# Kernel optimization log

Hardware: AMD Instinct MI355X
Metric: run time of the kernel (lower is better)

The kernel has to match this reference:

```python
import jax, jax.numpy as jnp
import numpy as np

B, N, D_IN = 4, 2048, 128
H, HD = 4, 32  # num_heads, head_dim (out_features=128, concat=True)
NEG_SLOPE = 0.2


def setup_inputs() -> dict:
    key = jax.random.key(0)
    kx, kadj, kw, ka = jax.random.split(key, 4)
    x = jax.random.normal(kx, (B, N, D_IN), dtype=jnp.float32)
    adj_mx = jax.random.randint(kadj, (N, N), 0, 2, dtype=jnp.int32)
    # xavier-uniform-ish scaling for params
    W = jax.random.normal(kw, (H * HD, D_IN), dtype=jnp.float32) * (1.0 / np.sqrt(D_IN))
    a = jax.random.normal(ka, (H, 2 * HD, 1), dtype=jnp.float32) * (1.0 / np.sqrt(2 * HD))
    return {"x": x, "adj_mx": adj_mx, "W": W, "a": a}


def reference(x, adj_mx, W, a):
    # x: (B,N,D_in); W: (H*hd, D_in) [nn.Linear weight]; a: (H, 2*hd, 1)
    b, n, _ = x.shape
    hd = a.shape[1] // 2
    h = (x @ W.T).reshape(b, n, H, hd)  # (B,N,H,hd)
    # e_ij = a^T [h_i || h_j] = a1.h_i + a2.h_j  (exact decomposition of the concat-matmul)
    a1 = a[:, :hd, 0]  # (H, hd)
    a2 = a[:, hd:, 0]  # (H, hd)
    ei = jnp.einsum('bnhd,hd->bnh', h, a1)
    ej = jnp.einsum('bnhd,hd->bnh', h, a2)
    e = ei[:, :, None, :] + ej[:, None, :, :]  # (B,N,N,H)
    e = jnp.where(e > 0, e, NEG_SLOPE * e)  # leaky_relu(0.2)
    mask = (adj_mx == 0)[None, :, :, None]  # (1,N,N,1)
    e = jnp.where(mask, -jnp.inf, e)
    attn = jax.nn.softmax(e, axis=2)  # softmax over neighbors j
    # dropout p=0.0 (inference) -> identity
    out = jnp.einsum('bijh,bjhd->bihd', attn, h)  # (B,N,H,hd)
    return out.reshape(b, n, H * hd)  # concat heads
```

## Files before the change

### kernel.cpp

```cpp
#include <hip/hip_runtime.h>
#include <hip/hip_bf16.h>
#include <stdint.h>

#define B 4
#define N 2048
#define DIN 128
#define H 4
#define HD 32
#define NEG 0.2f

typedef __attribute__((ext_vector_type(8))) short short8;
typedef __attribute__((ext_vector_type(4))) float f32x4;

__global__ __launch_bounds__(256) void k_gemm(const float* __restrict__ x,
                                              const float* __restrict__ W,
                                              const float* __restrict__ a,
                                              unsigned short* __restrict__ VT,
                                              float* __restrict__ ei_t,
                                              float* __restrict__ ej_t) {
    __shared__ float Wt0[64][64];
    __shared__ float Wt1[64][64];
    __shared__ float xT[64][20];
    const int tid = threadIdx.x;
    const int lane = tid & 63;
    const int r0 = (tid >> 6) * 4;
    const int c2 = lane;
    const int rowBase = blockIdx.x * 16;
    float acc[4][2];
#pragma unroll
    for (int i = 0; i < 4; ++i) { acc[i][0] = 0.f; acc[i][1] = 0.f; }

    for (int kh = 0; kh < 2; ++kh) {
        __syncthreads();
        {
            const int c = tid & 127;
            const int qb = (tid >> 7) * 8;
            const int ci = c >> 1, pl = c & 1;
            const float4* W4 = (const float4*)W;
#pragma unroll
            for (int q = 0; q < 8; ++q) {
                float4 v = W4[c * 32 + kh * 16 + qb + q];
                int kk = (qb + q) * 4;
                if (pl == 0) {
                    Wt0[kk + 0][ci] = v.x; Wt0[kk + 1][ci] = v.y;
                    Wt0[kk + 2][ci] = v.z; Wt0[kk + 3][ci] = v.w;
                } else {
                    Wt1[kk + 0][ci] = v.x; Wt1[kk + 1][ci] = v.y;
                    Wt1[kk + 2][ci] = v.z; Wt1[kk + 3][ci] = v.w;
                }
            }
        }
        {
            const int rl = tid >> 4;
            const int q = tid & 15;
            float4 v = ((const float4*)x)[(rowBase + rl) * 32 + kh * 16 + q];
            int kk = q * 4;
            xT[kk + 0][rl] = v.x; xT[kk + 1][rl] = v.y;
            xT[kk + 2][rl] = v.z; xT[kk + 3][rl] = v.w;
        }
        __syncthreads();
#pragma unroll 8
        for (int kk = 0; kk < 64; ++kk) {
            float w0 = Wt0[kk][c2];
            float w1 = Wt1[kk][c2];
#pragma unroll
            for (int i = 0; i < 4; ++i) {
                float xv = xT[kk][r0 + i];
                acc[i][0] += xv * w0;
                acc[i][1] += xv * w1;
            }
        }
    }

    const int c0 = 2 * c2;
    const int head = c0 >> 5, d0 = c0 & 31;
    const int b = rowBase >> 11;
    const int n0 = (rowBase & 2047) + r0;
    const int bh = b * 4 + head;

    {
        ushort4 p0, p1;
        unsigned short* q0 = (unsigned short*)&p0;
        unsigned short* q1 = (unsigned short*)&p1;
#pragma unroll
        for (int i = 0; i < 4; ++i) {
            __hip_bfloat16 h0 = __float2bfloat16(acc[i][0]);
            __hip_bfloat16 h1 = __float2bfloat16(acc[i][1]);
            q0[i] = *(unsigned short*)&h0;
            q1[i] = *(unsigned short*)&h1;
        }
        *(ushort4*)&VT[((size_t)bh * 32 + d0) * 2048 + n0] = p0;
        *(ushort4*)&VT[((size_t)bh * 32 + d0 + 1) * 2048 + n0] = p1;
    }
    {
        float a10 = a[head * 64 + d0],      a11 = a[head * 64 + d0 + 1];
        float a20 = a[head * 64 + 32 + d0], a21 = a[head * 64 + 32 + d0 + 1];
#pragma unroll
        for (int i = 0; i < 4; ++i) {
            float pi = acc[i][0] * a10 + acc[i][1] * a11;
            float pj = acc[i][0] * a20 + acc[i][1] * a21;
#pragma unroll
            for (int off = 1; off < 16; off <<= 1) {
                pi += __shfl_xor(pi, off);
                pj += __shfl_xor(pj, off);
            }
            if ((lane & 15) == 0) {
                ei_t[(size_t)bh * 2048 + n0 + i] = pi;
                ej_t[(size_t)bh * 2048 + n0 + i] = pj;
            }
        }
    }
}

__global__ __launch_bounds__(256) void k_pack(const int* __restrict__ adj,
                                              unsigned long long* __restrict__ bits) {
    int t = blockIdx.x * 256 + threadIdx.x;
    int v = adj[t];
    unsigned long long m = __ballot(v != 0);
    if ((threadIdx.x & 63) == 0) bits[t >> 6] = m;
}

__global__ __launch_bounds__(512) void k_attn_g(const unsigned short* __restrict__ VT,
                                                const float* __restrict__ ei_t,
                                                const float* __restrict__ ej_t,
                                                const unsigned long long* __restrict__ bits,
                                                float* __restrict__ out) {
    __shared__ float red[4][64][13];

    const int tid = threadIdx.x;
    const int bid = blockIdx.x;
    const int rt = bid & 31;
    const int head = (bid >> 5) & 3;
    const int b = bid >> 7;
    const int wv = tid >> 6, lane = tid & 63;
    const int wtile = wv & 3, par = wv >> 2;
    const int lr = lane & 15;
    const int g = lane >> 4;
    const int rowW = rt * 64 + wtile * 16;
    const int bh = b * 4 + head;

    const unsigned short* V0 = VT + (size_t)bh * 32 * 2048 + (size_t)lr * 2048;
    const unsigned short* V1 = V0 + 16 * 2048;
    const float* ejp = ej_t + (size_t)bh * 2048;
    const float eir = ei_t[(size_t)bh * 2048 + rowW + lr];
    const unsigned long long* mrow = bits + (size_t)(rowW + lr) * (N / 64);

    f32x4 acc0 = {0.f, 0.f, 0.f, 0.f};
    f32x4 acc1 = {0.f, 0.f, 0.f, 0.f};
    f32x4 accS = {0.f, 0.f, 0.f, 0.f};
    short8 onesb;
    {
        short ov = (lr == 0) ? (short)0x3F80 : (short)0;
#pragma unroll
        for (int e = 0; e < 8; ++e) onesb[e] = ov;
    }

    for (int jc = par * 64; jc < N; jc += 128) {
        const unsigned long long word = mrow[jc >> 6];
#pragma unroll
        for (int ks = 0; ks < 2; ++ks) {
            const int joff = jc + ks * 32 + g * 8;
            float4 ea = *(const float4*)(ejp + joff);
            float4 eb = *(const float4*)(ejp + joff + 4);
            short8 b0 = *(const short8*)(V0 + joff);
            short8 b1 = *(const short8*)(V1 + joff);
            const unsigned int mb = (unsigned int)(word >> (ks * 32 + g * 8)) & 0xffu;
            float ej8[8] = {ea.x, ea.y, ea.z, ea.w, eb.x, eb.y, eb.z, eb.w};
            short8 pa;
#pragma unroll
            for (int e = 0; e < 8; ++e) {
                float s = eir + ej8[e];
                float el = fmaxf(s, NEG * s);
                float p = ((mb >> e) & 1u) ? __expf(el) : 0.f;
                __hip_bfloat16 pb = __float2bfloat16(p);
                pa[e] = (short)*(unsigned short*)&pb;
            }
            acc0 = __builtin_amdgcn_mfma_f32_16x16x32_bf16(pa, b0, acc0, 0, 0, 0);
            acc1 = __builtin_amdgcn_mfma_f32_16x16x32_bf16(pa, b1, acc1, 0, 0, 0);
            accS = __builtin_amdgcn_mfma_f32_16x16x32_bf16(pa, onesb, accS, 0, 0, 0);
        }
    }

    if (par == 1) {
        float* r = &red[wtile][lane][0];
#pragma unroll
        for (int q = 0; q < 4; ++q) {
            r[q] = acc0[q]; r[4 + q] = acc1[q]; r[8 + q] = accS[q];
        }
    }
    __syncthreads();
    if (par == 0) {
        const float* r = &red[wtile][lane][0];
#pragma unroll
        for (int q = 0; q < 4; ++q) {
            acc0[q] += r[q]; acc1[q] += r[4 + q]; accS[q] += r[8 + q];
        }
#pragma unroll
        for (int reg = 0; reg < 4; ++reg) {
            const float sr = __shfl(accS[reg], g * 16);
            const float inv = 1.f / sr;
            const int m = 4 * g + reg;
            float* dst = &out[(size_t)(b * N + rowW + m) * 128 + head * 32 + lr];
            dst[0]  = acc0[reg] * inv;
            dst[16] = acc1[reg] * inv;
        }
    }
}

__global__ __launch_bounds__(256) void k_fused(const float* __restrict__ x,
                                               const int* __restrict__ adj,
                                               const float* __restrict__ W,
                                               const float* __restrict__ a,
                                               float* __restrict__ out) {
    __shared__ float Ws[32][129];
    __shared__ float xs[64][132];
    __shared__ float hs[64][44];
    __shared__ float ejs[64];
    __shared__ float eis[128];
    __shared__ float a1s[32], a2s[32];
    __shared__ unsigned long long mb[128];

    const int tid = threadIdx.x;
    const int bid = blockIdx.x;
    const int rt = bid & 15;
    const int head = (bid >> 4) & 3;
    const int b = bid >> 6;
    const int row0 = rt * 128;

    for (int idx = tid; idx < 32 * 128; idx += 256) {
        int d = idx >> 7, k = idx & 127;
        Ws[d][k] = W[(head * 32 + d) * 128 + k];
    }
    if (tid < 32) a1s[tid] = a[head * 64 + tid];
    else if (tid < 64) a2s[tid - 32] = a[head * 64 + tid];
    __syncthreads();

    for (int c0 = 0; c0 < 128; c0 += 64) {
        __syncthreads();
        {
            int jj = tid >> 2, k0 = (tid & 3) * 32;
            const float4* src = (const float4*)&x[(b * N + row0 + c0 + jj) * 128 + k0];
#pragma unroll
            for (int q = 0; q < 8; ++q) *(float4*)&xs[jj][k0 + q * 4] = src[q];
        }
        __syncthreads();
        {
            int jj = tid >> 2, db = (tid & 3) * 8;
#pragma unroll
            for (int dd = 0; dd < 8; ++dd) {
                float s = 0.f;
                for (int k = 0; k < 128; ++k) s += xs[jj][k] * Ws[db + dd][k];
                hs[jj][db + dd] = s;
            }
        }
        __syncthreads();
        if (tid < 64) {
            float s = 0.f;
#pragma unroll
            for (int d = 0; d < 32; ++d) s += hs[tid][d] * a1s[d];
            eis[c0 + tid] = s;
        }
    }

    const int dgrp = tid & 3, d0 = dgrp * 8;
    const int rseg = tid >> 2;
    float acc[2][8];
    float sacc[2] = {0.f, 0.f};
#pragma unroll
    for (int k = 0; k < 2; ++k)
#pragma unroll
        for (int d = 0; d < 8; ++d) acc[k][d] = 0.f;

    for (int jc = 0; jc < N; jc += 64) {
        __syncthreads();
        {
            int jj = tid >> 2, k0 = (tid & 3) * 32;
            const float4* src = (const float4*)&x[(b * N + jc + jj) * 128 + k0];
#pragma unroll
            for (int q = 0; q < 8; ++q) *(float4*)&xs[jj][k0 + q * 4] = src[q];
        }
        {
            int wv = tid >> 6, lane = tid & 63;
            for (int p = 0; p < 32; ++p) {
                int il = p * 4 + wv;
                unsigned long long m = __ballot(adj[(row0 + il) * N + jc + lane] != 0);
                if (lane == 0) mb[il] = m;
            }
        }
        __syncthreads();
        {
            int jj = tid >> 2, db = (tid & 3) * 8;
#pragma unroll
            for (int dd = 0; dd < 8; ++dd) {
                float s = 0.f;
                for (int k = 0; k < 128; ++k) s += xs[jj][k] * Ws[db + dd][k];
                hs[jj][db + dd] = s;
            }
        }
        __syncthreads();
        if (tid < 64) {
            float s = 0.f;
#pragma unroll
            for (int d = 0; d < 32; ++d) s += hs[tid][d] * a2s[d];
            ejs[tid] = s;
        }
        __syncthreads();
        for (int jj = 0; jj < 64; ++jj) {
            float ejv = ejs[jj];
            float hv[8];
#pragma unroll
            for (int d = 0; d < 8; ++d) hv[d] = hs[jj][d0 + d];
#pragma unroll
            for (int k = 0; k < 2; ++k) {
                int il = rseg * 2 + k;
                float s = eis[il] + ejv;
                float el = s > 0.f ? s : NEG * s;
                float p = ((mb[il] >> jj) & 1ull) ? __expf(el) : 0.f;
                sacc[k] += p;
#pragma unroll
                for (int d = 0; d < 8; ++d) acc[k][d] += p * hv[d];
            }
        }
    }
#pragma unroll
    for (int k = 0; k < 2; ++k) {
        int il = rseg * 2 + k;
        float inv = 1.f / sacc[k];
        float* dst = &out[(b * N + row0 + il) * 128 + head * 32 + d0];
#pragma unroll
        for (int d = 0; d < 8; ++d) dst[d] = acc[k][d] * inv;
    }
}

extern "C" void kernel_launch(void* const* d_in, const int* in_sizes, int n_in,
                              void* d_out, int out_size, void* d_ws, size_t ws_size,
                              hipStream_t stream) {
    const float* x = nullptr; const int* adj = nullptr;
    const float* W = nullptr; const float* a = nullptr;
    for (int i = 0; i < n_in; ++i) {
        switch (in_sizes[i]) {
            case B * N * DIN:  x   = (const float*)d_in[i]; break;
            case N * N:        adj = (const int*)d_in[i];   break;
            case H * HD * DIN: W   = (const float*)d_in[i]; break;
            case H * 2 * HD:   a   = (const float*)d_in[i]; break;
        }
    }
    float* out = (float*)d_out;

    const size_t szVT = (size_t)B * H * HD * N * 2;
    const size_t szE  = (size_t)B * H * N * 4;
    const size_t szBits = (size_t)N * (N / 64) * 8;
    const size_t need = szVT + 2 * szE + szBits;

    if (ws_size >= need) {
        char* ws = (char*)d_ws;
        unsigned short* VT = (unsigned short*)ws;
        float* ei_t = (float*)(ws + szVT);
        float* ej_t = (float*)(ws + szVT + szE);
        unsigned long long* bits = (unsigned long long*)(ws + szVT + 2 * szE);

        k_gemm<<<512, 256, 0, stream>>>(x, W, a, VT, ei_t, ej_t);
        k_pack<<<(N * N) / 256, 256, 0, stream>>>(adj, bits);
        k_attn_g<<<512, 512, 0, stream>>>(VT, ei_t, ej_t, bits, out);
    } else {
        k_fused<<<256, 256, 0, stream>>>(x, adj, W, a, out);
    }
}
```

Before: 130.5 us.

## Split attention kernel over four j-partitions with register double-buffered loads and exp2

The attention kernel now gives each block 32 rows, using two row tiles times four j-partitions per 512-thread block, and launches twice as many blocks. The j loop is software-pipelined: the mask word and V tiles for the next chunk are loaded into registers while the current chunk is computed. ei/ej are pre-scaled by log2(e) in the GEMM kernel so the inner loop can use exp2 directly. The aim is more parallelism, hidden load latency and cheaper exponentials, at the cost of a larger three-way LDS reduction and extra register pressure.

New measurement: 130.1 us. No clear change (-0.3%).

```diff
diff --git a/kernel.cpp b/kernel.cpp
--- a/kernel.cpp
+++ b/kernel.cpp
@@ -8,6 +8,7 @@
 #define H 4
 #define HD 32
 #define NEG 0.2f
+#define LOG2E 1.4426950408889634f
 
 typedef __attribute__((ext_vector_type(8))) short short8;
 typedef __attribute__((ext_vector_type(4))) float f32x4;
@@ -105,8 +106,8 @@
                 pj += __shfl_xor(pj, off);
             }
             if ((lane & 15) == 0) {
-                ei_t[(size_t)bh * 2048 + n0 + i] = pi;
-                ej_t[(size_t)bh * 2048 + n0 + i] = pj;
+                ei_t[(size_t)bh * 2048 + n0 + i] = pi * LOG2E;
+                ej_t[(size_t)bh * 2048 + n0 + i] = pj * LOG2E;
             }
         }
     }
@@ -125,18 +126,18 @@
                                                 const float* __restrict__ ej_t,
                                                 const unsigned long long* __restrict__ bits,
                                                 float* __restrict__ out) {
-    __shared__ float red[4][64][13];
+    __shared__ float red[3][2][64][13];
 
     const int tid = threadIdx.x;
     const int bid = blockIdx.x;
-    const int rt = bid & 31;
-    const int head = (bid >> 5) & 3;
-    const int b = bid >> 7;
+    const int rt = bid & 63;
+    const int head = (bid >> 6) & 3;
+    const int b = bid >> 8;
     const int wv = tid >> 6, lane = tid & 63;
-    const int wtile = wv & 3, par = wv >> 2;
+    const int wtile = wv & 1, par = wv >> 1;
     const int lr = lane & 15;
     const int g = lane >> 4;
-    const int rowW = rt * 64 + wtile * 16;
+    const int rowW = rt * 32 + wtile * 16;
     const int bh = b * 4 + head;
 
     const unsigned short* V0 = VT + (size_t)bh * 32 * 2048 + (size_t)lr * 2048;
@@ -155,15 +156,23 @@
         for (int e = 0; e < 8; ++e) onesb[e] = ov;
     }
 
-    for (int jc = par * 64; jc < N; jc += 128) {
-        const unsigned long long word = mrow[jc >> 6];
+    const int jstart = par * 64;
+
+    auto LDC = [&](int jc, unsigned long long& w,
+                   short8& v00, short8& v10, short8& v01, short8& v11) {
+        w = mrow[jc >> 6];
+        v00 = *(const short8*)(V0 + jc + g * 8);
+        v10 = *(const short8*)(V1 + jc + g * 8);
+        v01 = *(const short8*)(V0 + jc + 32 + g * 8);
+        v11 = *(const short8*)(V1 + jc + 32 + g * 8);
+    };
+    auto CMP = [&](int jc, unsigned long long word,
+                   short8 v00, short8 v10, short8 v01, short8 v11) {
 #pragma unroll
         for (int ks = 0; ks < 2; ++ks) {
             const int joff = jc + ks * 32 + g * 8;
             float4 ea = *(const float4*)(ejp + joff);
             float4 eb = *(const float4*)(ejp + joff + 4);
-            short8 b0 = *(const short8*)(V0 + joff);
-            short8 b1 = *(const short8*)(V1 + joff);
             const unsigned int mb = (unsigned int)(word >> (ks * 32 + g * 8)) & 0xffu;
             float ej8[8] = {ea.x, ea.y, ea.z, ea.w, eb.x, eb.y, eb.z, eb.w};
             short8 pa;
@@ -171,18 +180,35 @@
             for (int e = 0; e < 8; ++e) {
                 float s = eir + ej8[e];
                 float el = fmaxf(s, NEG * s);
-                float p = ((mb >> e) & 1u) ? __expf(el) : 0.f;
+                float p = ((mb >> e) & 1u) ? __builtin_amdgcn_exp2f(el) : 0.f;
                 __hip_bfloat16 pb = __float2bfloat16(p);
                 pa[e] = (short)*(unsigned short*)&pb;
             }
-            acc0 = __builtin_amdgcn_mfma_f32_16x16x32_bf16(pa, b0, acc0, 0, 0, 0);
-            acc1 = __builtin_amdgcn_mfma_f32_16x16x32_bf16(pa, b1, acc1, 0, 0, 0);
+            short8 u0 = ks ? v01 : v00;
+            short8 u1 = ks ? v11 : v10;
+            acc0 = __builtin_amdgcn_mfma_f32_16x16x32_bf16(pa, u0, acc0, 0, 0, 0);
+            acc1 = __builtin_amdgcn_mfma_f32_16x16x32_bf16(pa, u1, acc1, 0, 0, 0);
             accS = __builtin_amdgcn_mfma_f32_16x16x32_bf16(pa, onesb, accS, 0, 0, 0);
         }
-    }
-
-    if (par == 1) {
-        float* r = &red[wtile][lane][0];
+    };
+
+    unsigned long long wA, wB;
+    short8 A00, A10, A01, A11, B00, B10, B01, B11;
+    int jc = jstart;
+    LDC(jc, wA, A00, A10, A01, A11);
+#pragma unroll 1
+    for (int it = 0; it < 4; ++it) {
+        int j1 = jc + 256; if (j1 >= N) j1 = jstart;
+        LDC(j1, wB, B00, B10, B01, B11);
+        CMP(jc, wA, A00, A10, A01, A11);
+        int j2 = j1 + 256; if (j2 >= N) j2 = jstart;
+        LDC(j2, wA, A00, A10, A01, A11);
+        CMP(j1, wB, B00, B10, B01, B11);
+        jc = j2;
+    }
+
+    if (par != 0) {
+        float* r = &red[par - 1][wtile][lane][0];
 #pragma unroll
         for (int q = 0; q < 4; ++q) {
             r[q] = acc0[q]; r[4 + q] = acc1[q]; r[8 + q] = accS[q];
@@ -190,10 +216,13 @@
     }
     __syncthreads();
     if (par == 0) {
-        const float* r = &red[wtile][lane][0];
-#pragma unroll
-        for (int q = 0; q < 4; ++q) {
-            acc0[q] += r[q]; acc1[q] += r[4 + q]; accS[q] += r[8 + q];
+#pragma unroll
+        for (int p = 0; p < 3; ++p) {
+            const float* r = &red[p][wtile][lane][0];
+#pragma unroll
+            for (int q = 0; q < 4; ++q) {
+                acc0[q] += r[q]; acc1[q] += r[4 + q]; accS[q] += r[8 + q];
+            }
         }
 #pragma unroll
         for (int reg = 0; reg < 4; ++reg) {
@@ -361,7 +390,7 @@
 
         k_gemm<<<512, 256, 0, stream>>>(x, W, a, VT, ei_t, ej_t);
         k_pack<<<(N * N) / 256, 256, 0, stream>>>(adj, bits);
-        k_attn_g<<<512, 512, 0, stream>>>(VT, ei_t, ej_t, bits, out);
+        k_attn_g<<<1024, 512, 0, stream>>>(VT, ei_t, ej_t, bits, out);
     } else {
         k_fused<<<256, 256, 0, stream>>>(x, adj, W, a, out);
     }
```

## Stage V and ej windows in LDS with double buffering and merge prep kernels

Applied to the files above, without the earlier changes.

Fuses the adjacency bit-pack kernel into the projection kernel as extra blocks, which removes one launch. The attention kernel now uses 128-row blocks (256 blocks) and stages 512-column windows of V (swizzled XOR layout written by the producer) and ej into double-buffered LDS. Global prefetch of the next window overlaps with MFMA compute, replacing per-wave direct global loads and the two-half partial reduction. The exponent is switched to exp2 with log2e folded into ei/ej. The trade-off is fewer blocks, which means lower parallelism on the large CU count.

Measured after the change: 111.7 us. -14.4%, faster.

```diff
diff --git a/kernel.cpp b/kernel.cpp
--- a/kernel.cpp
+++ b/kernel.cpp
@@ -8,20 +8,33 @@
 #define H 4
 #define HD 32
 #define NEG 0.2f
+#define LOG2E 1.4426950408889634f
+#define WINJ 512
 
 typedef __attribute__((ext_vector_type(8))) short short8;
 typedef __attribute__((ext_vector_type(4))) float f32x4;
 
-__global__ __launch_bounds__(256) void k_gemm(const float* __restrict__ x,
+__global__ __launch_bounds__(256) void k_prep(const float* __restrict__ x,
                                               const float* __restrict__ W,
                                               const float* __restrict__ a,
+                                              const int* __restrict__ adj,
                                               unsigned short* __restrict__ VT,
                                               float* __restrict__ ei_t,
-                                              float* __restrict__ ej_t) {
+                                              float* __restrict__ ej_t,
+                                              unsigned long long* __restrict__ bits) {
     __shared__ float Wt0[64][64];
     __shared__ float Wt1[64][64];
     __shared__ float xT[64][20];
+
     const int tid = threadIdx.x;
+    if (blockIdx.x >= 512) {
+        int t = (blockIdx.x - 512) * 256 + tid;
+        int v = adj[t];
+        unsigned long long m = __ballot(v != 0);
+        if ((tid & 63) == 0) bits[t >> 6] = m;
+        return;
+    }
+
     const int lane = tid & 63;
     const int r0 = (tid >> 6) * 4;
     const int c2 = lane;
@@ -89,8 +102,13 @@
             q0[i] = *(unsigned short*)&h0;
             q1[i] = *(unsigned short*)&h1;
         }
-        *(ushort4*)&VT[((size_t)bh * 32 + d0) * 2048 + n0] = p0;
-        *(ushort4*)&VT[((size_t)bh * 32 + d0 + 1) * 2048 + n0] = p1;
+        const int wdw = n0 >> 9;
+        const int gw  = (n0 >> 3) & 63;
+        const int off = n0 & 7;
+        const int gs0 = gw ^ (d0 & 7);
+        const int gs1 = gw ^ ((d0 + 1) & 7);
+        *(ushort4*)&VT[((size_t)bh * 32 + d0) * 2048 + wdw * WINJ + gs0 * 8 + off] = p0;
+        *(ushort4*)&VT[((size_t)bh * 32 + d0 + 1) * 2048 + wdw * WINJ + gs1 * 8 + off] = p1;
     }
     {
         float a10 = a[head * 64 + d0],      a11 = a[head * 64 + d0 + 1];
@@ -105,43 +123,34 @@
                 pj += __shfl_xor(pj, off);
             }
             if ((lane & 15) == 0) {
-                ei_t[(size_t)bh * 2048 + n0 + i] = pi;
-                ej_t[(size_t)bh * 2048 + n0 + i] = pj;
+                ei_t[(size_t)bh * 2048 + n0 + i] = pi * LOG2E;
+                ej_t[(size_t)bh * 2048 + n0 + i] = pj * LOG2E;
             }
         }
     }
 }
 
-__global__ __launch_bounds__(256) void k_pack(const int* __restrict__ adj,
-                                              unsigned long long* __restrict__ bits) {
-    int t = blockIdx.x * 256 + threadIdx.x;
-    int v = adj[t];
-    unsigned long long m = __ballot(v != 0);
-    if ((threadIdx.x & 63) == 0) bits[t >> 6] = m;
-}
-
-__global__ __launch_bounds__(512) void k_attn_g(const unsigned short* __restrict__ VT,
+__global__ __launch_bounds__(512) void k_attn_l(const unsigned short* __restrict__ VT,
                                                 const float* __restrict__ ei_t,
                                                 const float* __restrict__ ej_t,
                                                 const unsigned long long* __restrict__ bits,
                                                 float* __restrict__ out) {
-    __shared__ float red[4][64][13];
+    __shared__ unsigned short Vs[2][32 * WINJ];
+    __shared__ float ejs[2][WINJ];
 
     const int tid = threadIdx.x;
     const int bid = blockIdx.x;
-    const int rt = bid & 31;
-    const int head = (bid >> 5) & 3;
-    const int b = bid >> 7;
+    const int rt = bid & 15;
+    const int head = (bid >> 4) & 3;
+    const int b = bid >> 6;
     const int wv = tid >> 6, lane = tid & 63;
-    const int wtile = wv & 3, par = wv >> 2;
     const int lr = lane & 15;
     const int g = lane >> 4;
-    const int rowW = rt * 64 + wtile * 16;
+    const int rowW = rt * 128 + wv * 16;
     const int bh = b * 4 + head;
 
-    const unsigned short* V0 = VT + (size_t)bh * 32 * 2048 + (size_t)lr * 2048;
-    const unsigned short* V1 = V0 + 16 * 2048;
-    const float* ejp = ej_t + (size_t)bh * 2048;
+    const unsigned short* VTb = VT + (size_t)bh * 32 * 2048;
+    const float* ejg = ej_t + (size_t)bh * 2048;
     const float eir = ei_t[(size_t)bh * 2048 + rowW + lr];
     const unsigned long long* mrow = bits + (size_t)(rowW + lr) * (N / 64);
 
@@ -155,55 +164,89 @@
         for (int e = 0; e < 8; ++e) onesb[e] = ov;
     }
 
-    for (int jc = par * 64; jc < N; jc += 128) {
-        const unsigned long long word = mrow[jc >> 6];
-#pragma unroll
-        for (int ks = 0; ks < 2; ++ks) {
-            const int joff = jc + ks * 32 + g * 8;
-            float4 ea = *(const float4*)(ejp + joff);
-            float4 eb = *(const float4*)(ejp + joff + 4);
-            short8 b0 = *(const short8*)(V0 + joff);
-            short8 b1 = *(const short8*)(V1 + joff);
-            const unsigned int mb = (unsigned int)(word >> (ks * 32 + g * 8)) & 0xffu;
-            float ej8[8] = {ea.x, ea.y, ea.z, ea.w, eb.x, eb.y, eb.z, eb.w};
-            short8 pa;
-#pragma unroll
-            for (int e = 0; e < 8; ++e) {
-                float s = eir + ej8[e];
-                float el = fmaxf(s, NEG * s);
-                float p = ((mb >> e) & 1u) ? __expf(el) : 0.f;
-                __hip_bfloat16 pb = __float2bfloat16(p);
-                pa[e] = (short)*(unsigned short*)&pb;
-            }
-            acc0 = __builtin_amdgcn_mfma_f32_16x16x32_bf16(pa, b0, acc0, 0, 0, 0);
-            acc1 = __builtin_amdgcn_mfma_f32_16x16x32_bf16(pa, b1, acc1, 0, 0, 0);
-            accS = __builtin_amdgcn_mfma_f32_16x16x32_bf16(pa, onesb, accS, 0, 0, 0);
-        }
-    }
-
-    if (par == 1) {
-        float* r = &red[wtile][lane][0];
-#pragma unroll
-        for (int q = 0; q < 4; ++q) {
-            r[q] = acc0[q]; r[4 + q] = acc1[q]; r[8 + q] = accS[q];
+    {
+#pragma unroll
+        for (int i = 0; i < 4; ++i) {
+            int L = i * 512 + tid, d = L >> 6, gr = L & 63;
+            float4 v = *(const float4*)&VTb[(size_t)d * 2048 + gr * 8];
+            *(float4*)&Vs[0][(size_t)L * 8] = v;
+        }
+        if (tid < 128) {
+            float4 e = *(const float4*)&ejg[tid * 4];
+            *(float4*)&ejs[0][tid * 4] = e;
         }
     }
     __syncthreads();
-    if (par == 0) {
-        const float* r = &red[wtile][lane][0];
-#pragma unroll
-        for (int q = 0; q < 4; ++q) {
-            acc0[q] += r[q]; acc1[q] += r[4 + q]; accS[q] += r[8 + q];
-        }
-#pragma unroll
-        for (int reg = 0; reg < 4; ++reg) {
-            const float sr = __shfl(accS[reg], g * 16);
-            const float inv = 1.f / sr;
-            const int m = 4 * g + reg;
-            float* dst = &out[(size_t)(b * N + rowW + m) * 128 + head * 32 + lr];
-            dst[0]  = acc0[reg] * inv;
-            dst[16] = acc1[reg] * inv;
-        }
+
+    for (int w = 0; w < 4; ++w) {
+        const int buf = w & 1;
+        float4 vr0, vr1, vr2, vr3, er;
+        const bool pf = (w < 3);
+        if (pf) {
+            const unsigned short* src = VTb + (w + 1) * WINJ;
+            int L0 = tid,        d0_ = L0 >> 6, g0_ = L0 & 63;
+            int L1 = 512 + tid,  d1_ = L1 >> 6, g1_ = L1 & 63;
+            int L2 = 1024 + tid, d2_ = L2 >> 6, g2_ = L2 & 63;
+            int L3 = 1536 + tid, d3_ = L3 >> 6, g3_ = L3 & 63;
+            vr0 = *(const float4*)&src[(size_t)d0_ * 2048 + g0_ * 8];
+            vr1 = *(const float4*)&src[(size_t)d1_ * 2048 + g1_ * 8];
+            vr2 = *(const float4*)&src[(size_t)d2_ * 2048 + g2_ * 8];
+            vr3 = *(const float4*)&src[(size_t)d3_ * 2048 + g3_ * 8];
+            if (tid < 128) er = *(const float4*)&ejg[(w + 1) * WINJ + tid * 4];
+        }
+        __builtin_amdgcn_sched_barrier(0);
+
+        const unsigned short* Vb = &Vs[buf][0];
+        const float* ejb = &ejs[buf][0];
+#pragma unroll 4
+        for (int jl = 0; jl < WINJ; jl += 64) {
+            const unsigned long long word = mrow[(w * WINJ + jl) >> 6];
+#pragma unroll
+            for (int ks = 0; ks < 2; ++ks) {
+                const int G = (jl >> 3) + ks * 4 + g;
+                const int gs = (G ^ (lr & 7)) * 8;
+                short8 b0 = *(const short8*)&Vb[lr * WINJ + gs];
+                short8 b1 = *(const short8*)&Vb[(16 + lr) * WINJ + gs];
+                const int f = jl + ks * 32 + g * 8;
+                float4 ea = *(const float4*)&ejb[f];
+                float4 eb = *(const float4*)&ejb[f + 4];
+                const unsigned int mb =
+                    (unsigned int)(word >> (ks * 32 + g * 8)) & 0xffu;
+                float ej8[8] = {ea.x, ea.y, ea.z, ea.w, eb.x, eb.y, eb.z, eb.w};
+                short8 pa;
+#pragma unroll
+                for (int e = 0; e < 8; ++e) {
+                    float s = eir + ej8[e];
+                    float el = fmaxf(s, NEG * s);
+                    float p = ((mb >> e) & 1u) ? __builtin_amdgcn_exp2f(el) : 0.f;
+                    __hip_bfloat16 pb = __float2bfloat16(p);
+                    pa[e] = (short)*(unsigned short*)&pb;
+                }
+                acc0 = __builtin_amdgcn_mfma_f32_16x16x32_bf16(pa, b0, acc0, 0, 0, 0);
+                acc1 = __builtin_amdgcn_mfma_f32_16x16x32_bf16(pa, b1, acc1, 0, 0, 0);
+                accS = __builtin_amdgcn_mfma_f32_16x16x32_bf16(pa, onesb, accS, 0, 0, 0);
+            }
+        }
+
+        if (pf) {
+            const int nbuf = buf ^ 1;
+            *(float4*)&Vs[nbuf][(size_t)tid * 8]          = vr0;
+            *(float4*)&Vs[nbuf][(size_t)(512 + tid) * 8]  = vr1;
+            *(float4*)&Vs[nbuf][(size_t)(1024 + tid) * 8] = vr2;
+            *(float4*)&Vs[nbuf][(size_t)(1536 + tid) * 8] = vr3;
+            if (tid < 128) *(float4*)&ejs[nbuf][tid * 4] = er;
+        }
+        __syncthreads();
+    }
+
+#pragma unroll
+    for (int reg = 0; reg < 4; ++reg) {
+        const float sr = __shfl(accS[reg], g * 16);
+        const float inv = 1.f / sr;
+        const int m = 4 * g + reg;
+        float* dst = &out[(size_t)(b * N + rowW + m) * 128 + head * 32 + lr];
+        dst[0]  = acc0[reg] * inv;
+        dst[16] = acc1[reg] * inv;
     }
 }
 
@@ -359,9 +402,8 @@
         float* ej_t = (float*)(ws + szVT + szE);
         unsigned long long* bits = (unsigned long long*)(ws + szVT + 2 * szE);
 
-        k_gemm<<<512, 256, 0, stream>>>(x, W, a, VT, ei_t, ej_t);
-        k_pack<<<(N * N) / 256, 256, 0, stream>>>(adj, bits);
-        k_attn_g<<<512, 512, 0, stream>>>(VT, ei_t, ej_t, bits, out);
+        k_prep<<<512 + (N * N) / 256, 256, 0, stream>>>(x, W, a, adj, VT, ei_t, ej_t, bits);
+        k_attn_l<<<256, 512, 0, stream>>>(VT, ei_t, ej_t, bits, out);
     } else {
         k_fused<<<256, 256, 0, stream>>>(x, adj, W, a, out);
     }
```

## Fuse adjacency packing into GEMM, tile V layout, prefetch V fragments

Applied to the files above, without the earlier changes.

Merges the adjacency bit-packing kernel into the projection kernel as extra blocks, which saves one launch. V is now written through shared memory into a fragment-tiled layout so each MFMA operand is a contiguous 16-byte load, replacing the earlier strided rows. The attention loop software-prefetches the next iteration's V fragments and mask word. It also folds log2(e) into ei/ej so the kernel can use native exp2. The changes cost extra shared memory, registers and occupancy-hint constraints, and the loop is now hardcoded to 16 iterations.

New measurement: 116.1 us. -11.0%, faster.

```diff
diff --git a/kernel.cpp b/kernel.cpp
--- a/kernel.cpp
+++ b/kernel.cpp
@@ -8,20 +8,34 @@
 #define H 4
 #define HD 32
 #define NEG 0.2f
+#define LOG2E 1.4426950408889634f
 
 typedef __attribute__((ext_vector_type(8))) short short8;
 typedef __attribute__((ext_vector_type(4))) float f32x4;
 
-__global__ __launch_bounds__(256) void k_gemm(const float* __restrict__ x,
+
+__global__ __launch_bounds__(256) void k_prep(const float* __restrict__ x,
                                               const float* __restrict__ W,
                                               const float* __restrict__ a,
+                                              const int* __restrict__ adj,
                                               unsigned short* __restrict__ VT,
                                               float* __restrict__ ei_t,
-                                              float* __restrict__ ej_t) {
+                                              float* __restrict__ ej_t,
+                                              unsigned long long* __restrict__ bits) {
     __shared__ float Wt0[64][64];
     __shared__ float Wt1[64][64];
     __shared__ float xT[64][20];
+    __shared__ unsigned short Vl[16][128];
+
     const int tid = threadIdx.x;
+    if (blockIdx.x >= 512) {
+        int t = (blockIdx.x - 512) * 256 + tid;
+        int v = adj[t];
+        unsigned long long m = __ballot(v != 0);
+        if ((tid & 63) == 0) bits[t >> 6] = m;
+        return;
+    }
+
     const int lane = tid & 63;
     const int r0 = (tid >> 6) * 4;
     const int c2 = lane;
@@ -73,28 +87,26 @@
     }
 
     const int c0 = 2 * c2;
-    const int head = c0 >> 5, d0 = c0 & 31;
+    const int headT = c0 >> 5, d0 = c0 & 31;
     const int b = rowBase >> 11;
     const int n0 = (rowBase & 2047) + r0;
-    const int bh = b * 4 + head;
+    const int n0_blk = rowBase & 2047;
 
     {
-        ushort4 p0, p1;
-        unsigned short* q0 = (unsigned short*)&p0;
-        unsigned short* q1 = (unsigned short*)&p1;
+        unsigned int* Vl32 = (unsigned int*)&Vl[0][0];
 #pragma unroll
         for (int i = 0; i < 4; ++i) {
             __hip_bfloat16 h0 = __float2bfloat16(acc[i][0]);
             __hip_bfloat16 h1 = __float2bfloat16(acc[i][1]);
-            q0[i] = *(unsigned short*)&h0;
-            q1[i] = *(unsigned short*)&h1;
-        }
-        *(ushort4*)&VT[((size_t)bh * 32 + d0) * 2048 + n0] = p0;
-        *(ushort4*)&VT[((size_t)bh * 32 + d0 + 1) * 2048 + n0] = p1;
+            unsigned int v = (unsigned int)*(unsigned short*)&h0 |
+                             ((unsigned int)*(unsigned short*)&h1 << 16);
+            Vl32[(r0 + i) * 64 + c2] = v;
+        }
     }
     {
-        float a10 = a[head * 64 + d0],      a11 = a[head * 64 + d0 + 1];
-        float a20 = a[head * 64 + 32 + d0], a21 = a[head * 64 + 32 + d0 + 1];
+        float a10 = a[headT * 64 + d0],      a11 = a[headT * 64 + d0 + 1];
+        float a20 = a[headT * 64 + 32 + d0], a21 = a[headT * 64 + 32 + d0 + 1];
+        const int bh_e = b * 4 + headT;
 #pragma unroll
         for (int i = 0; i < 4; ++i) {
             float pi = acc[i][0] * a10 + acc[i][1] * a11;
@@ -105,26 +117,35 @@
                 pj += __shfl_xor(pj, off);
             }
             if ((lane & 15) == 0) {
-                ei_t[(size_t)bh * 2048 + n0 + i] = pi;
-                ej_t[(size_t)bh * 2048 + n0 + i] = pj;
-            }
-        }
+                ei_t[(size_t)bh_e * 2048 + n0 + i] = pi * LOG2E;
+                ej_t[(size_t)bh_e * 2048 + n0 + i] = pj * LOG2E;
+            }
+        }
+    }
+    __syncthreads();
+    {
+        const int d = tid >> 1, nh = tid & 1;
+        const int hd_ = d >> 5, d31 = d & 31;
+        const int bh = b * 4 + hd_;
+        const int gran = (n0_blk >> 3) + nh;
+        ushort4 o0, o1;
+        unsigned short* q = (unsigned short*)&o0;
+#pragma unroll
+        for (int k = 0; k < 4; ++k) q[k] = Vl[nh * 8 + k][d];
+        q = (unsigned short*)&o1;
+#pragma unroll
+        for (int k = 0; k < 4; ++k) q[k] = Vl[nh * 8 + 4 + k][d];
+        unsigned short* dst = &VT[((size_t)(bh * 256 + gran) * 32 + d31) * 8];
+        *(ushort4*)&dst[0] = o0;
+        *(ushort4*)&dst[4] = o1;
     }
 }
 
-__global__ __launch_bounds__(256) void k_pack(const int* __restrict__ adj,
-                                              unsigned long long* __restrict__ bits) {
-    int t = blockIdx.x * 256 + threadIdx.x;
-    int v = adj[t];
-    unsigned long long m = __ballot(v != 0);
-    if ((threadIdx.x & 63) == 0) bits[t >> 6] = m;
-}
-
-__global__ __launch_bounds__(512) void k_attn_g(const unsigned short* __restrict__ VT,
-                                                const float* __restrict__ ei_t,
-                                                const float* __restrict__ ej_t,
-                                                const unsigned long long* __restrict__ bits,
-                                                float* __restrict__ out) {
+__global__ __launch_bounds__(512, 4) void k_attn_c(const unsigned short* __restrict__ VT,
+                                                   const float* __restrict__ ei_t,
+                                                   const float* __restrict__ ej_t,
+                                                   const unsigned long long* __restrict__ bits,
+                                                   float* __restrict__ out) {
     __shared__ float red[4][64][13];
 
     const int tid = threadIdx.x;
@@ -139,8 +160,7 @@
     const int rowW = rt * 64 + wtile * 16;
     const int bh = b * 4 + head;
 
-    const unsigned short* V0 = VT + (size_t)bh * 32 * 2048 + (size_t)lr * 2048;
-    const unsigned short* V1 = V0 + 16 * 2048;
+    const unsigned short* VTb = VT + (size_t)bh * 256 * 32 * 8;
     const float* ejp = ej_t + (size_t)bh * 2048;
     const float eir = ei_t[(size_t)bh * 2048 + rowW + lr];
     const unsigned long long* mrow = bits + (size_t)(rowW + lr) * (N / 64);
@@ -155,30 +175,47 @@
         for (int e = 0; e < 8; ++e) onesb[e] = ov;
     }
 
-    for (int jc = par * 64; jc < N; jc += 128) {
-        const unsigned long long word = mrow[jc >> 6];
+    auto FR = [&](int j32, int dbase) -> const short8* {
+        return (const short8*)&VTb[((size_t)(((j32) >> 3) + g) * 32 + dbase + lr) * 8];
+    };
+
+    int jc = par * 64;
+    unsigned long long wA = mrow[jc >> 6];
+    short8 a00 = *FR(jc, 0),      a10 = *FR(jc, 16);
+    short8 a01 = *FR(jc + 32, 0), a11 = *FR(jc + 32, 16);
+
+#pragma unroll 1
+    for (int it = 0; it < 16; ++it) {
+        int jn = jc + 128; if (jn >= N) jn = par * 64;
+        unsigned long long wB = mrow[jn >> 6];
+        short8 n00 = *FR(jn, 0),      n10 = *FR(jn, 16);
+        short8 n01 = *FR(jn + 32, 0), n11 = *FR(jn + 32, 16);
+        __builtin_amdgcn_sched_barrier(0);
+
 #pragma unroll
         for (int ks = 0; ks < 2; ++ks) {
             const int joff = jc + ks * 32 + g * 8;
-            float4 ea = *(const float4*)(ejp + joff);
-            float4 eb = *(const float4*)(ejp + joff + 4);
-            short8 b0 = *(const short8*)(V0 + joff);
-            short8 b1 = *(const short8*)(V1 + joff);
-            const unsigned int mb = (unsigned int)(word >> (ks * 32 + g * 8)) & 0xffu;
+            float4 ea = *(const float4*)&ejp[joff];
+            float4 eb = *(const float4*)&ejp[joff + 4];
+            const unsigned int mb = (unsigned int)(wA >> (ks * 32 + g * 8)) & 0xffu;
             float ej8[8] = {ea.x, ea.y, ea.z, ea.w, eb.x, eb.y, eb.z, eb.w};
             short8 pa;
 #pragma unroll
             for (int e = 0; e < 8; ++e) {
                 float s = eir + ej8[e];
                 float el = fmaxf(s, NEG * s);
-                float p = ((mb >> e) & 1u) ? __expf(el) : 0.f;
+                float p = ((mb >> e) & 1u) ? __builtin_amdgcn_exp2f(el) : 0.f;
                 __hip_bfloat16 pb = __float2bfloat16(p);
                 pa[e] = (short)*(unsigned short*)&pb;
             }
-            acc0 = __builtin_amdgcn_mfma_f32_16x16x32_bf16(pa, b0, acc0, 0, 0, 0);
-            acc1 = __builtin_amdgcn_mfma_f32_16x16x32_bf16(pa, b1, acc1, 0, 0, 0);
+            short8 u0 = ks ? a01 : a00;
+            short8 u1 = ks ? a11 : a10;
+            acc0 = __builtin_amdgcn_mfma_f32_16x16x32_bf16(pa, u0, acc0, 0, 0, 0);
+            acc1 = __builtin_amdgcn_mfma_f32_16x16x32_bf16(pa, u1, acc1, 0, 0, 0);
             accS = __builtin_amdgcn_mfma_f32_16x16x32_bf16(pa, onesb, accS, 0, 0, 0);
         }
+        wA = wB; a00 = n00; a10 = n10; a01 = n01; a11 = n11;
+        jc = jn;
     }
 
     if (par == 1) {
@@ -359,9 +396,8 @@
         float* ej_t = (float*)(ws + szVT + szE);
         unsigned long long* bits = (unsigned long long*)(ws + szVT + 2 * szE);
 
-        k_gemm<<<512, 256, 0, stream>>>(x, W, a, VT, ei_t, ej_t);
-        k_pack<<<(N * N) / 256, 256, 0, stream>>>(adj, bits);
-        k_attn_g<<<512, 512, 0, stream>>>(VT, ei_t, ej_t, bits, out);
+        k_prep<<<512 + (N * N) / 256, 256, 0, stream>>>(x, W, a, adj, VT, ei_t, ej_t, bits);
+        k_attn_c<<<512, 512, 0, stream>>>(VT, ei_t, ej_t, bits, out);
     } else {
         k_fused<<<256, 256, 0, stream>>>(x, adj, W, a, out);
     }
```
